# Optimization experiments

Hardware: AMD Instinct MI355X
Metric: run time of the kernel (lower is better)

Reference implementation:

```python
import jax, jax.numpy as jnp
import numpy as np

NUM_CHUNKS = 8
TOP_K = 2
IN_FEATURES = 4096
OUT_FEATURES = 4096
CIN = IN_FEATURES // NUM_CHUNKS    # 512
COUT = OUT_FEATURES // NUM_CHUNKS  # 512
BATCH = 8192


def setup_inputs() -> dict:
    key = jax.random.key(0)
    kx, kw, kb = jax.random.split(key, 3)
    x = jax.random.normal(kx, (BATCH, IN_FEATURES), dtype=jnp.float32)
    # per-chunk Linear params: W[i] is [out_chunk, in_chunk] like nn.Linear.weight
    bound = 1.0 / np.sqrt(CIN)
    W = jax.random.uniform(kw, (NUM_CHUNKS, COUT, CIN), jnp.float32, -bound, bound)
    b = jax.random.uniform(kb, (NUM_CHUNKS, COUT), jnp.float32, -bound, bound)
    return {"x": x, "W": W, "b": b}


def reference(x, W, b):
    B = x.shape[0]
    nc, cout, cin = W.shape
    # split into equal chunks along feature dim: [B, nc, cin]
    xr = x.reshape(B, nc, cin)
    # per-chunk activity: mean |x| over batch and chunk features -> [nc]
    activities = jnp.mean(jnp.abs(xr), axis=(0, 2))
    # select top-k most active chunks (indices are constants w.r.t. grads)
    _, idx = jax.lax.top_k(activities, TOP_K)  # [k]
    xs = xr[:, idx, :]                          # [B, k, cin]
    # grouped GEMM only on selected chunks: y = x @ W^T + b
    ys = jnp.einsum('bki,koi->bko', xs, W[idx]) + b[idx][None]  # [B, k, cout]
    out = jnp.zeros((B, nc, cout), dtype=x.dtype).at[:, idx, :].set(ys)
    return out.reshape(B, nc * cout), activities
```

## Files before the change

### kernel.cpp

```cpp
#include <hip/hip_runtime.h>
#include <hip/hip_bf16.h>

#define BATCH 8192
#define NCH 8
#define CIN 512
#define COUT 512
#define NF 4096

typedef __attribute__((ext_vector_type(8))) __bf16 bf16x8;
typedef __attribute__((ext_vector_type(4))) float f32x4;

__device__ __forceinline__ void async_load16(const void* g, void* l) {
    __builtin_amdgcn_global_load_lds((const __attribute__((address_space(1))) void*)g,
                                     (__attribute__((address_space(3))) void*)l, 16, 0, 0);
}

__device__ __forceinline__ bf16x8 cvt8(const float4 a, const float4 b) {
    bf16x8 p;
    p[0] = (__bf16)a.x; p[1] = (__bf16)a.y; p[2] = (__bf16)a.z; p[3] = (__bf16)a.w;
    p[4] = (__bf16)b.x; p[5] = (__bf16)b.y; p[6] = (__bf16)b.z; p[7] = (__bf16)b.w;
    return p;
}

__device__ __forceinline__ void recompute_top2(const float* __restrict__ partials,
                                               float* asums ,
                                               int& i0, int& i1) {
    const int t = threadIdx.x;
    const int c = t >> 5;
    const int j = t & 31;
    float p = 0.f;
#pragma unroll
    for (int k = 0; k < 8; ++k) p += partials[c * 256 + j * 8 + k];
#pragma unroll
    for (int off = 16; off > 0; off >>= 1) p += __shfl_down(p, off, 32);
    if (j == 0) asums[c] = p;
    __syncthreads();
    float a[NCH];
#pragma unroll
    for (int i = 0; i < NCH; ++i) a[i] = asums[i];
    i0 = 0;
#pragma unroll
    for (int i = 1; i < NCH; ++i) if (a[i] > a[i0]) i0 = i;
    i1 = (i0 == 0) ? 1 : 0;
#pragma unroll
    for (int i = 0; i < NCH; ++i) if (i != i0 && a[i] > a[i1]) i1 = i;
}

__global__ __launch_bounds__(256) void act_kernel(const float* __restrict__ x,
                                                  float* __restrict__ partials) {
    const int c = blockIdx.y;
    const int bx = blockIdx.x;
    const int t = threadIdx.x;
    const int wv = t >> 6;
    const int col = (t & 63) * 8;
    const size_t rbase = (size_t)bx * 32;
    float s = 0.f;
#pragma unroll
    for (int p = 0; p < 8; ++p) {
        const size_t r = rbase + p * 4 + wv;
        const float* src = x + r * NF + c * CIN + col;
        const float4 a0 = *(const float4*)(src);
        const float4 a1 = *(const float4*)(src + 4);
        s += fabsf(a0.x) + fabsf(a0.y) + fabsf(a0.z) + fabsf(a0.w)
           + fabsf(a1.x) + fabsf(a1.y) + fabsf(a1.z) + fabsf(a1.w);
    }
#pragma unroll
    for (int off = 32; off > 0; off >>= 1) s += __shfl_down(s, off, 64);
    __shared__ float red[4];
    const int lane = t & 63;
    if (lane == 0) red[wv] = s;
    __syncthreads();
    if (t == 0) partials[c * 256 + bx] = red[0] + red[1] + red[2] + red[3];
}

__global__ __launch_bounds__(256) void cvt_kernel(const float* __restrict__ x,
                                                  const float* __restrict__ W,
                                                  const float* __restrict__ partials,
                                                  __bf16* __restrict__ xc,
                                                  __bf16* __restrict__ wc,
                                                  float* __restrict__ out_act) {
    __shared__ float asums[NCH];
    int i0, i1;
    recompute_top2(partials, asums, i0, i1);

    const int z = blockIdx.y;
    const int c = (z == 0) ? i0 : i1;
    const int bx = blockIdx.x;
    const int t = threadIdx.x;

    if (bx == 0 && z == 0 && t < NCH)
        out_act[t] = asums[t] * (1.0f / ((float)BATCH * (float)CIN));

    if (bx >= 256) {
        const int q = bx - 256;
        const float* src = W + (size_t)c * (COUT * CIN) + q * 32768;
        __bf16* dst = wc + (size_t)z * (COUT * CIN) + q * 32768;
#pragma unroll
        for (int p = 0; p < 16; ++p) {
            const int off = p * 2048 + t * 8;
            const float4 a0 = *(const float4*)(src + off);
            const float4 a1 = *(const float4*)(src + off + 4);
            *(bf16x8*)(dst + off) = cvt8(a0, a1);
        }
        return;
    }

    const int wv = t >> 6;
    const int col = (t & 63) * 8;
    const size_t rbase = (size_t)bx * 32;
    __bf16* dst = xc + (size_t)z * BATCH * CIN;
#pragma unroll
    for (int p = 0; p < 8; ++p) {
        const size_t r = rbase + p * 4 + wv;
        const float* src = x + r * NF + c * CIN + col;
        const float4 a0 = *(const float4*)(src);
        const float4 a1 = *(const float4*)(src + 4);
        *(bf16x8*)(dst + r * CIN + col) = cvt8(a0, a1);
    }
}

__global__ __launch_bounds__(256) void gemm_kernel(const __bf16* __restrict__ xc,
                                                   const __bf16* __restrict__ wc,
                                                   const float* __restrict__ bias,
                                                   const float* __restrict__ partials,
                                                   float* __restrict__ out) {
    __shared__ float asums[NCH];
    int i0, i1;
    recompute_top2(partials, asums, i0, i1);

    const int c = blockIdx.z;
    const int t = threadIdx.x;
    const size_t obase = (size_t)(blockIdx.x * 128) * NF + c * COUT + blockIdx.y * 128;

    if (c != i0 && c != i1) {
        const float4 z = make_float4(0.f, 0.f, 0.f, 0.f);
        const int rq = t >> 5;
        const int cq = (t & 31) << 2;
#pragma unroll
        for (int p = 0; p < 16; ++p)
            *(float4*)(out + obase + (size_t)(p * 8 + rq) * NF + cq) = z;
        return;
    }
    const int kz = (c == i0) ? 0 : 1;

    __shared__ __bf16 Xs[128 * 32];
    __shared__ __bf16 Wsh[128 * 32];

    const int lane = t & 63, w = t >> 6;
    const int wm = (w >> 1) * 64, wn = (w & 1) * 64;
    const int lr = lane & 15, lq = lane >> 4;

    const int srow = lane >> 2;
    const int skcol = (lane & 3) * 8;
    const __bf16* xg = xc + (size_t)kz * BATCH * CIN
                     + (size_t)(blockIdx.x * 128 + w * 32 + srow) * CIN + skcol;
    const __bf16* wg = wc + (size_t)kz * COUT * CIN
                     + (size_t)(blockIdx.y * 128 + w * 32 + srow) * CIN + skcol;
    __bf16* xls = &Xs[(w * 32) * 32];
    __bf16* wls = &Wsh[(w * 32) * 32];

    f32x4 acc[4][4];
#pragma unroll
    for (int i = 0; i < 4; ++i)
#pragma unroll
        for (int j = 0; j < 4; ++j) acc[i][j] = (f32x4){0.f, 0.f, 0.f, 0.f};

    for (int kk = 0; kk < CIN; kk += 32) {
        async_load16(xg + kk, xls);
        async_load16(xg + kk + (size_t)16 * CIN, xls + 16 * 32);
        async_load16(wg + kk, wls);
        async_load16(wg + kk + (size_t)16 * CIN, wls + 16 * 32);
        __syncthreads();

        bf16x8 av[4], bv[4];
#pragma unroll
        for (int mt = 0; mt < 4; ++mt) av[mt] = *(const bf16x8*)&Xs[(wm + mt * 16 + lr) * 32 + lq * 8];
#pragma unroll
        for (int nt = 0; nt < 4; ++nt) bv[nt] = *(const bf16x8*)&Wsh[(wn + nt * 16 + lr) * 32 + lq * 8];
#pragma unroll
        for (int mt = 0; mt < 4; ++mt)
#pragma unroll
            for (int nt = 0; nt < 4; ++nt)
                acc[mt][nt] = __builtin_amdgcn_mfma_f32_16x16x32_bf16(av[mt], bv[nt], acc[mt][nt], 0, 0, 0);
        __syncthreads();
    }

    float bvv[4];
#pragma unroll
    for (int nt = 0; nt < 4; ++nt)
        bvv[nt] = bias[c * COUT + blockIdx.y * 128 + wn + nt * 16 + lr];
#pragma unroll
    for (int mt = 0; mt < 4; ++mt)
#pragma unroll
        for (int nt = 0; nt < 4; ++nt)
#pragma unroll
            for (int r = 0; r < 4; ++r) {
                const int row = wm + mt * 16 + lq * 4 + r;
                const int col = wn + nt * 16 + lr;
                out[obase + (size_t)row * NF + col] = acc[mt][nt][r] + bvv[nt];
            }
}

extern "C" void kernel_launch(void* const* d_in, const int* in_sizes, int n_in,
                              void* d_out, int out_size, void* d_ws, size_t ws_size,
                              hipStream_t stream) {
    const float* x = (const float*)d_in[0];
    const float* W = (const float*)d_in[1];
    const float* b = (const float*)d_in[2];
    float* out = (float*)d_out;

    float* partials = (float*)d_ws;
    __bf16* xc = (__bf16*)((char*)d_ws + 32768);
    __bf16* wc = (__bf16*)((char*)d_ws + 32768 + (size_t)2 * BATCH * CIN * 2);

    act_kernel<<<dim3(256, NCH), 256, 0, stream>>>(x, partials);
    cvt_kernel<<<dim3(264, 2), 256, 0, stream>>>(x, W, partials, xc, wc,
                                                 out + (size_t)BATCH * NF);
    gemm_kernel<<<dim3(64, 4, NCH), 256, 0, stream>>>(xc, wc, b, partials, out);
}
```

Before: 271.6 us.

## Fuse fp32-to-bf16 conversion into GEMM with register-prefetched global loads

Drops the separate conversion kernel, which wrote bf16 copies of the selected x chunks and weights to workspace. The GEMM now reads fp32 x and W directly, converts them in registers and stores the result to LDS. The next k-tile is loaded into registers while the MFMAs run on the current one. This saves one launch and the bf16 round trip through memory, but each GEMM block re-reads fp32 data (twice the bytes) across the 4 N-tiles and uses more registers.

```diff
diff --git a/kernel.cpp b/kernel.cpp
--- a/kernel.cpp
+++ b/kernel.cpp
@@ -9,11 +9,6 @@
 
 typedef __attribute__((ext_vector_type(8))) __bf16 bf16x8;
 typedef __attribute__((ext_vector_type(4))) float f32x4;
-
-__device__ __forceinline__ void async_load16(const void* g, void* l) {
-    __builtin_amdgcn_global_load_lds((const __attribute__((address_space(1))) void*)g,
-                                     (__attribute__((address_space(3))) void*)l, 16, 0, 0);
-}
 
 __device__ __forceinline__ bf16x8 cvt8(const float4 a, const float4 b) {
     bf16x8 p;
@@ -73,57 +68,12 @@
     if (t == 0) partials[c * 256 + bx] = red[0] + red[1] + red[2] + red[3];
 }
 
-__global__ __launch_bounds__(256) void cvt_kernel(const float* __restrict__ x,
-                                                  const float* __restrict__ W,
-                                                  const float* __restrict__ partials,
-                                                  __bf16* __restrict__ xc,
-                                                  __bf16* __restrict__ wc,
-                                                  float* __restrict__ out_act) {
-    __shared__ float asums[NCH];
-    int i0, i1;
-    recompute_top2(partials, asums, i0, i1);
-
-    const int z = blockIdx.y;
-    const int c = (z == 0) ? i0 : i1;
-    const int bx = blockIdx.x;
-    const int t = threadIdx.x;
-
-    if (bx == 0 && z == 0 && t < NCH)
-        out_act[t] = asums[t] * (1.0f / ((float)BATCH * (float)CIN));
-
-    if (bx >= 256) {
-        const int q = bx - 256;
-        const float* src = W + (size_t)c * (COUT * CIN) + q * 32768;
-        __bf16* dst = wc + (size_t)z * (COUT * CIN) + q * 32768;
-#pragma unroll
-        for (int p = 0; p < 16; ++p) {
-            const int off = p * 2048 + t * 8;
-            const float4 a0 = *(const float4*)(src + off);
-            const float4 a1 = *(const float4*)(src + off + 4);
-            *(bf16x8*)(dst + off) = cvt8(a0, a1);
-        }
-        return;
-    }
-
-    const int wv = t >> 6;
-    const int col = (t & 63) * 8;
-    const size_t rbase = (size_t)bx * 32;
-    __bf16* dst = xc + (size_t)z * BATCH * CIN;
-#pragma unroll
-    for (int p = 0; p < 8; ++p) {
-        const size_t r = rbase + p * 4 + wv;
-        const float* src = x + r * NF + c * CIN + col;
-        const float4 a0 = *(const float4*)(src);
-        const float4 a1 = *(const float4*)(src + 4);
-        *(bf16x8*)(dst + r * CIN + col) = cvt8(a0, a1);
-    }
-}
-
-__global__ __launch_bounds__(256) void gemm_kernel(const __bf16* __restrict__ xc,
-                                                   const __bf16* __restrict__ wc,
-                                                   const float* __restrict__ bias,
-                                                   const float* __restrict__ partials,
-                                                   float* __restrict__ out) {
+__global__ __launch_bounds__(256) void fused_kernel(const float* __restrict__ x,
+                                                    const float* __restrict__ W,
+                                                    const float* __restrict__ bias,
+                                                    const float* __restrict__ partials,
+                                                    float* __restrict__ out,
+                                                    float* __restrict__ out_act) {
     __shared__ float asums[NCH];
     int i0, i1;
     recompute_top2(partials, asums, i0, i1);
@@ -131,6 +81,9 @@
     const int c = blockIdx.z;
     const int t = threadIdx.x;
     const size_t obase = (size_t)(blockIdx.x * 128) * NF + c * COUT + blockIdx.y * 128;
+
+    if (blockIdx.x == 0 && blockIdx.y == 0 && c == 0 && t < NCH)
+        out_act[t] = asums[t] * (1.0f / ((float)BATCH * (float)CIN));
 
     if (c != i0 && c != i1) {
         const float4 z = make_float4(0.f, 0.f, 0.f, 0.f);
@@ -141,7 +94,6 @@
             *(float4*)(out + obase + (size_t)(p * 8 + rq) * NF + cq) = z;
         return;
     }
-    const int kz = (c == i0) ? 0 : 1;
 
     __shared__ __bf16 Xs[128 * 32];
     __shared__ __bf16 Wsh[128 * 32];
@@ -150,14 +102,18 @@
     const int wm = (w >> 1) * 64, wn = (w & 1) * 64;
     const int lr = lane & 15, lq = lane >> 4;
 
-    const int srow = lane >> 2;
-    const int skcol = (lane & 3) * 8;
-    const __bf16* xg = xc + (size_t)kz * BATCH * CIN
-                     + (size_t)(blockIdx.x * 128 + w * 32 + srow) * CIN + skcol;
-    const __bf16* wg = wc + (size_t)kz * COUT * CIN
-                     + (size_t)(blockIdx.y * 128 + w * 32 + srow) * CIN + skcol;
-    __bf16* xls = &Xs[(w * 32) * 32];
-    __bf16* wls = &Wsh[(w * 32) * 32];
+    const int r0 = t >> 2;
+    const int k0 = (t & 3) * 8;
+
+    const float* xg0 = x + (size_t)(blockIdx.x * 128 + r0) * NF + c * CIN + k0;
+    const float* xg1 = xg0 + (size_t)64 * NF;
+    const float* wg0 = W + (size_t)c * (COUT * CIN)
+                     + (size_t)(blockIdx.y * 128 + r0) * CIN + k0;
+    const float* wg1 = wg0 + (size_t)64 * CIN;
+    __bf16* xs0 = &Xs[r0 * 32 + k0];
+    __bf16* xs1 = xs0 + 64 * 32;
+    __bf16* ws0 = &Wsh[r0 * 32 + k0];
+    __bf16* ws1 = ws0 + 64 * 32;
 
     f32x4 acc[4][4];
 #pragma unroll
@@ -165,25 +121,45 @@
 #pragma unroll
         for (int j = 0; j < 4; ++j) acc[i][j] = (f32x4){0.f, 0.f, 0.f, 0.f};
 
-    for (int kk = 0; kk < CIN; kk += 32) {
-        async_load16(xg + kk, xls);
-        async_load16(xg + kk + (size_t)16 * CIN, xls + 16 * 32);
-        async_load16(wg + kk, wls);
-        async_load16(wg + kk + (size_t)16 * CIN, wls + 16 * 32);
+    float4 a0, a1, a2, a3, b0, b1, b2, b3;
+
+#define LOADK(off) \
+    a0 = *(const float4*)(xg0 + (off));     a1 = *(const float4*)(xg0 + (off) + 4); \
+    a2 = *(const float4*)(xg1 + (off));     a3 = *(const float4*)(xg1 + (off) + 4); \
+    b0 = *(const float4*)(wg0 + (off));     b1 = *(const float4*)(wg0 + (off) + 4); \
+    b2 = *(const float4*)(wg1 + (off));     b3 = *(const float4*)(wg1 + (off) + 4);
+
+#define STAGE() \
+    *(bf16x8*)xs0 = cvt8(a0, a1); *(bf16x8*)xs1 = cvt8(a2, a3); \
+    *(bf16x8*)ws0 = cvt8(b0, b1); *(bf16x8*)ws1 = cvt8(b2, b3);
+
+#define COMPUTE() { \
+    bf16x8 av[4], bv[4]; \
+    _Pragma("unroll") \
+    for (int mt = 0; mt < 4; ++mt) av[mt] = *(const bf16x8*)&Xs[(wm + mt * 16 + lr) * 32 + lq * 8]; \
+    _Pragma("unroll") \
+    for (int nt = 0; nt < 4; ++nt) bv[nt] = *(const bf16x8*)&Wsh[(wn + nt * 16 + lr) * 32 + lq * 8]; \
+    _Pragma("unroll") \
+    for (int mt = 0; mt < 4; ++mt) \
+    _Pragma("unroll") \
+    for (int nt = 0; nt < 4; ++nt) \
+        acc[mt][nt] = __builtin_amdgcn_mfma_f32_16x16x32_bf16(av[mt], bv[nt], acc[mt][nt], 0, 0, 0); }
+
+    LOADK(0);
+    for (int kk = 0; kk < CIN - 32; kk += 32) {
+        STAGE();
         __syncthreads();
-
-        bf16x8 av[4], bv[4];
-#pragma unroll
-        for (int mt = 0; mt < 4; ++mt) av[mt] = *(const bf16x8*)&Xs[(wm + mt * 16 + lr) * 32 + lq * 8];
-#pragma unroll
-        for (int nt = 0; nt < 4; ++nt) bv[nt] = *(const bf16x8*)&Wsh[(wn + nt * 16 + lr) * 32 + lq * 8];
-#pragma unroll
-        for (int mt = 0; mt < 4; ++mt)
-#pragma unroll
-            for (int nt = 0; nt < 4; ++nt)
-                acc[mt][nt] = __builtin_amdgcn_mfma_f32_16x16x32_bf16(av[mt], bv[nt], acc[mt][nt], 0, 0, 0);
+        LOADK(kk + 32);
+        COMPUTE();
         __syncthreads();
     }
+    STAGE();
+    __syncthreads();
+    COMPUTE();
+
+#undef LOADK
+#undef STAGE
+#undef COMPUTE
 
     float bvv[4];
 #pragma unroll
@@ -210,11 +186,8 @@
     float* out = (float*)d_out;
 
     float* partials = (float*)d_ws;
-    __bf16* xc = (__bf16*)((char*)d_ws + 32768);
-    __bf16* wc = (__bf16*)((char*)d_ws + 32768 + (size_t)2 * BATCH * CIN * 2);
 
     act_kernel<<<dim3(256, NCH), 256, 0, stream>>>(x, partials);
-    cvt_kernel<<<dim3(264, 2), 256, 0, stream>>>(x, W, partials, xc, wc,
-                                                 out + (size_t)BATCH * NF);
-    gemm_kernel<<<dim3(64, 4, NCH), 256, 0, stream>>>(xc, wc, b, partials, out);
+    fused_kernel<<<dim3(64, 4, NCH), 256, 0, stream>>>(x, W, b, partials, out,
+                                                       out + (size_t)BATCH * NF);
 }
```

Result: no change. 272.2 us (+0.2%).
